# Kernel tuning notes

Measured on AMD Instinct MI355X. Metric: run time of the kernel, lower is better.

The kernel has to match this reference:

```python
import jax, jax.numpy as jnp
import numpy as np

N_POINTS = 300000
NUM_CLUSTERS = 64
LATENT_DIM = 32
DET = 1e-16  # matches `det` in update_gamma


def setup_inputs() -> dict:
    key = jax.random.key(0)
    k1, k2, k3 = jax.random.split(key, 3)
    mu_phi = jax.random.normal(k1, (N_POINTS, LATENT_DIM), dtype=jnp.float32)
    # per-node scalar log-variance (encoder's gcn_logstddev has output dim 1)
    log_cov_phi = jax.random.normal(k2, (N_POINTS, 1), dtype=jnp.float32) * 0.1
    pi_k = jnp.ones((NUM_CLUSTERS,), jnp.float32) / NUM_CLUSTERS
    mu_k = jax.random.normal(k3, (NUM_CLUSTERS, LATENT_DIM), dtype=jnp.float32)
    log_cov_k = jnp.full((NUM_CLUSTERS, 1), 0.1, jnp.float32)
    return {"mu_phi": mu_phi, "log_cov_phi": log_cov_phi, "pi_k": pi_k,
            "mu_k": mu_k, "log_cov_k": log_cov_k, "P": LATENT_DIM}


def _sq_dist(a, b):
    # ||a_i - b_k||^2 via expansion; avoids materializing [N,K,P]
    return (jnp.sum(a * a, axis=1)[:, None]
            - 2.0 * (a @ b.T)
            + jnp.sum(b * b, axis=1)[None, :])


def reference(mu_phi, log_cov_phi, pi_k, mu_k, log_cov_k, P):
    Pf = jnp.float32(P)
    lcp = log_cov_phi[:, 0]          # [N]
    lck = log_cov_k[:, 0]            # [K]
    # --- update_gamma: KL[i,k] between q(z_i) and cluster k (isotropic) ---
    sq = _sq_dist(mu_phi, mu_k)      # [N,K]
    inv_cov_k = jnp.exp(-lck)[None, :]
    KL = 0.5 * (Pf * (lck[None, :] - lcp[:, None]) - Pf
                + Pf * jnp.exp(lcp)[:, None] * inv_cov_k
                + sq * inv_cov_k)    # [N,K]
    w = pi_k[None, :] * jnp.exp(-KL)
    gamma = w / jnp.sum(w, axis=1, keepdims=True) + DET  # [N,K]
    # --- update_others: M-step using the new gamma ---
    N_k = jnp.sum(gamma, axis=0)                          # [K]
    pi_new = N_k / jnp.float32(gamma.shape[0])
    mu_new = (gamma.T @ mu_phi) / N_k[:, None]            # [K,P]
    sq2 = _sq_dist(mu_phi, mu_new)                        # [N,K]
    diff = Pf * jnp.exp(lcp)[:, None] + sq2               # [N,K]
    cov_new = jnp.sum(gamma * diff, axis=0) / (Pf * N_k)  # [K]
    log_cov_new = jnp.log(cov_new)[:, None]               # [K,1]
    return gamma, pi_new, mu_new, log_cov_new
```

## Files before the change

### kernel.cpp

```cpp
#include <hip/hip_runtime.h>
#include <math.h>

#define NPTS 300000
#define K 64
#define P 32
#define DETC 1e-16f
#define WS_FLOATS (K + K + K * P)

#define NTHREADS 256
#define WPB (NTHREADS / 64)
#define NTILES ((NPTS + 63) / 64)
#define NBLOCKS ((NTILES + WPB - 1) / WPB)

#define DPP_ADD(v, ctrl)                                                     \
    v += __int_as_float(__builtin_amdgcn_update_dpp(                         \
        0, __float_as_int(v), (ctrl), 0xF, 0xF, true))

__device__ __forceinline__ float rlf(float x, int l) {
    return __int_as_float(__builtin_amdgcn_readlane(__float_as_int(x), l));
}

__device__ __forceinline__ float wave_sum64(float w) {
    float v = w;
    DPP_ADD(v, 0xB1);
    DPP_ADD(v, 0x4E);
    DPP_ADD(v, 0x128);
    DPP_ADD(v, 0x124);
    DPP_ADD(v, 0x142);
    DPP_ADD(v, 0x143);
    return rlf(v, 63);
}

__global__ __launch_bounds__(NTHREADS, 4) void em_pass(
    const float* __restrict__ mu_phi,
    const float* __restrict__ log_cov_phi,
    const float* __restrict__ pi_k,
    const float* __restrict__ mu_k,
    const float* __restrict__ log_cov_k,
    float* __restrict__ gamma_out,
    float* __restrict__ out_tail,
    float* __restrict__ ws)
{
    const int lane = threadIdx.x & 63;
    const int wave = threadIdx.x >> 6;
    const int tile = __builtin_amdgcn_readfirstlane(blockIdx.x * WPB + wave);

    float muk[P];
#pragma unroll
    for (int d = 0; d < P; ++d) muk[d] = mu_k[lane * P + d];
    const float lck  = log_cov_k[lane];
    const float icov = __expf(-lck);
    const float pik  = pi_k[lane];
    float n2k = 0.f;
#pragma unroll
    for (int d = 0; d < P; ++d) n2k = fmaf(muk[d], muk[d], n2k);
    const float Ak    = 0.5f * (32.f * lck - 32.f + icov * n2k) - __logf(pik);
    const float hicov = 0.5f * icov;

    float accN = 0.f, accS = 0.f;
    float accM[P];
#pragma unroll
    for (int d = 0; d < P; ++d) accM[d] = 0.f;

    if (tile < NTILES) {
        const int gb  = tile * 64;
        const int cnt = (NPTS - gb < 64) ? (NPTS - gb) : 64;

        const int ip = gb + ((lane < cnt) ? lane : (cnt - 1));
        float r[P];
        {
            const float4* r4 = reinterpret_cast<const float4*>(mu_phi + (size_t)ip * P);
            float4 a0 = r4[0], a1 = r4[1], a2 = r4[2], a3 = r4[3];
            float4 a4 = r4[4], a5 = r4[5], a6 = r4[6], a7 = r4[7];
#define PUT(j,q) r[4*j+0]=q.x; r[4*j+1]=q.y; r[4*j+2]=q.z; r[4*j+3]=q.w
            PUT(0,a0); PUT(1,a1); PUT(2,a2); PUT(3,a3);
            PUT(4,a4); PUT(5,a5); PUT(6,a6); PUT(7,a7);
#undef PUT
        }
        float n2 = 0.f;
#pragma unroll
        for (int d = 0; d < P; ++d) n2 = fmaf(r[d], r[d], n2);
        const float lcp = log_cov_phi[ip];
        const float u_v = fmaf(32.f, __expf(lcp), n2);
        const float b_v = 16.f * lcp;

        for (int p = 0; p < cnt; ++p) {
            float sr[P];
#pragma unroll
            for (int d = 0; d < P; ++d) sr[d] = rlf(r[d], p);

            float d0 = 0.f, d1 = 0.f, d2 = 0.f, d3 = 0.f;
#pragma unroll
            for (int d = 0; d < P; d += 4) {
                d0 = fmaf(sr[d + 0], muk[d + 0], d0);
                d1 = fmaf(sr[d + 1], muk[d + 1], d1);
                d2 = fmaf(sr[d + 2], muk[d + 2], d2);
                d3 = fmaf(sr[d + 3], muk[d + 3], d3);
            }
            const float dot = (d0 + d1) + (d2 + d3);

            const float u_s = rlf(u_v, p);
            const float b_s = rlf(b_v, p);
            const float t = fmaf(-hicov, u_s, b_s) - Ak;
            const float w = __expf(fmaf(icov, dot, t));

            const float s = wave_sum64(w);
            const float g = fmaf(w, __builtin_amdgcn_rcpf(s), DETC);
            gamma_out[(size_t)(gb + p) * K + lane] = g;

            accN += g;
            accS = fmaf(g, u_s, accS);
#pragma unroll
            for (int d = 0; d < P; ++d) accM[d] = fmaf(g, sr[d], accM[d]);
        }
    }

    __shared__ float lN[K], lS[K], lM[K * P];
    for (int idx = threadIdx.x; idx < K; idx += NTHREADS) { lN[idx] = 0.f; lS[idx] = 0.f; }
    for (int idx = threadIdx.x; idx < K * P; idx += NTHREADS) lM[idx] = 0.f;
    __syncthreads();

    atomicAdd(&lN[lane], accN);
    atomicAdd(&lS[lane], accS);
#pragma unroll
    for (int d = 0; d < P; ++d) atomicAdd(&lM[d * K + lane], accM[d]);
    __syncthreads();

    for (int idx = threadIdx.x; idx < K; idx += NTHREADS) {
        atomicAdd(&ws[idx], lN[idx]);
        atomicAdd(&ws[K + idx], lS[idx]);
    }
    for (int idx = threadIdx.x; idx < K * P; idx += NTHREADS)
        atomicAdd(&ws[2 * K + idx], lM[idx]);
    __syncthreads();

    __shared__ int lastf;
    if (threadIdx.x == 0) {
        __threadfence();
        const int c = atomicAdd((int*)(ws + WS_FLOATS), 1);
        lastf = (c == NBLOCKS - 1);
    }
    __syncthreads();
    if (lastf) {
        __threadfence();
        const int k = threadIdx.x;
        if (k < K) {
            const float Nk = __hip_atomic_load(&ws[k],     __ATOMIC_RELAXED, __HIP_MEMORY_SCOPE_AGENT);
            const float S  = __hip_atomic_load(&ws[K + k], __ATOMIC_RELAXED, __HIP_MEMORY_SCOPE_AGENT);
            float* pi_new      = out_tail;
            float* mu_new      = out_tail + K;
            float* log_cov_new = out_tail + K + K * P;

            pi_new[k] = Nk / (float)NPTS;
            const float invN = 1.f / Nk;
            float m2 = 0.f;
#pragma unroll
            for (int d = 0; d < P; ++d) {
                const float md = __hip_atomic_load(&ws[2 * K + d * K + k],
                                                   __ATOMIC_RELAXED, __HIP_MEMORY_SCOPE_AGENT) * invN;
                mu_new[k * P + d] = md;
                m2 = fmaf(md, md, m2);
            }
            const float cov = (S - Nk * m2) / (32.f * Nk);
            log_cov_new[k] = logf(cov);
        }
    }
}

extern "C" void kernel_launch(void* const* d_in, const int* in_sizes, int n_in,
                              void* d_out, int out_size, void* d_ws, size_t ws_size,
                              hipStream_t stream)
{
    const float* mu_phi      = (const float*)d_in[0];
    const float* log_cov_phi = (const float*)d_in[1];
    const float* pi_k        = (const float*)d_in[2];
    const float* mu_k        = (const float*)d_in[3];
    const float* log_cov_k   = (const float*)d_in[4];
    float* out = (float*)d_out;
    float* ws  = (float*)d_ws;

    hipMemsetAsync(ws, 0, (WS_FLOATS + 1) * sizeof(float), stream);
    em_pass<<<NBLOCKS, NTHREADS, 0, stream>>>(mu_phi, log_cov_phi, pi_k, mu_k,
                                              log_cov_k, out,
                                              out + (size_t)NPTS * K, ws);
}
```

Measured before the change: 216.2 us.

## Map one point per lane and transpose gamma through LDS for M-step accumulation

Each lane now owns one data point and loops over all 64 clusters, reading cluster means as wave-uniform values. This removes the per-point readlane broadcasts and the 64-lane DPP reduction of the old cluster-per-lane scheme. Gamma and the point features are staged in per-wave LDS and read back transposed, so each lane accumulates the N_k, covariance and mean sums for one cluster over half the points. The exponent is rewritten as a single exp2, and occupancy is lowered to 2 waves per SIMD to make room for the larger register footprint (w[64], accM[32]).

```diff
diff --git a/kernel.cpp b/kernel.cpp
--- a/kernel.cpp
+++ b/kernel.cpp
@@ -8,30 +8,27 @@
 #define WS_FLOATS (K + K + K * P)
 
 #define NTHREADS 256
-#define WPB (NTHREADS / 64)
+#define WPB 4
 #define NTILES ((NPTS + 63) / 64)
 #define NBLOCKS ((NTILES + WPB - 1) / WPB)
 
-#define DPP_ADD(v, ctrl)                                                     \
-    v += __int_as_float(__builtin_amdgcn_update_dpp(                         \
-        0, __float_as_int(v), (ctrl), 0xF, 0xF, true))
+#define PHS 36
+#define GS  33
+#define WAVE_LDS (64 * PHS + 64 * GS)
+#define COMB_OFF (WPB * WAVE_LDS)
+#define TOTAL_LDS (COMB_OFF + WS_FLOATS)
+
+#if __has_builtin(__builtin_amdgcn_exp2f)
+#define EXP2(x) __builtin_amdgcn_exp2f(x)
+#else
+#define EXP2(x) __exp2f(x)
+#endif
 
 __device__ __forceinline__ float rlf(float x, int l) {
     return __int_as_float(__builtin_amdgcn_readlane(__float_as_int(x), l));
 }
 
-__device__ __forceinline__ float wave_sum64(float w) {
-    float v = w;
-    DPP_ADD(v, 0xB1);
-    DPP_ADD(v, 0x4E);
-    DPP_ADD(v, 0x128);
-    DPP_ADD(v, 0x124);
-    DPP_ADD(v, 0x142);
-    DPP_ADD(v, 0x143);
-    return rlf(v, 63);
-}
-
-__global__ __launch_bounds__(NTHREADS, 4) void em_pass(
+__global__ __launch_bounds__(NTHREADS, 2) void em_pass(
     const float* __restrict__ mu_phi,
     const float* __restrict__ log_cov_phi,
     const float* __restrict__ pi_k,
@@ -41,104 +38,146 @@
     float* __restrict__ out_tail,
     float* __restrict__ ws)
 {
+    __shared__ float smem[TOTAL_LDS];
+    __shared__ int lastf;
+
     const int lane = threadIdx.x & 63;
     const int wave = threadIdx.x >> 6;
     const int tile = __builtin_amdgcn_readfirstlane(blockIdx.x * WPB + wave);
 
-    float muk[P];
-#pragma unroll
-    for (int d = 0; d < P; ++d) muk[d] = mu_k[lane * P + d];
-    const float lck  = log_cov_k[lane];
-    const float icov = __expf(-lck);
-    const float pik  = pi_k[lane];
-    float n2k = 0.f;
-#pragma unroll
-    for (int d = 0; d < P; ++d) n2k = fmaf(muk[d], muk[d], n2k);
-    const float Ak    = 0.5f * (32.f * lck - 32.f + icov * n2k) - __logf(pik);
-    const float hicov = 0.5f * icov;
-
-    float accN = 0.f, accS = 0.f;
+    float* phiT = smem + wave * WAVE_LDS;
+    float* G    = phiT + 64 * PHS;
+    float* comb = smem + COMB_OFF;
+
+    const float LOG2E = 1.4426950408889634f;
+
+    float icL, c2L;
+    {
+        const float4* mk4 = reinterpret_cast<const float4*>(mu_k + lane * P);
+        float n2k = 0.f;
+#pragma unroll
+        for (int q = 0; q < 8; ++q) {
+            float4 v = mk4[q];
+            n2k = fmaf(v.x, v.x, n2k); n2k = fmaf(v.y, v.y, n2k);
+            n2k = fmaf(v.z, v.z, n2k); n2k = fmaf(v.w, v.w, n2k);
+        }
+        const float lck  = log_cov_k[lane];
+        const float icov = __expf(-lck);
+        const float pik  = pi_k[lane];
+        const float C = fmaf(-0.5f * icov, n2k, 16.f - 16.f * lck) + __logf(pik);
+        icL = icov * LOG2E;
+        c2L = C * LOG2E;
+    }
+
+    for (int idx = threadIdx.x; idx < WS_FLOATS; idx += NTHREADS) comb[idx] = 0.f;
+    __syncthreads();
+
+    const int gb  = tile * 64;
+    const int cnt = (NPTS - gb < 64) ? (NPTS - gb) : 64;
+
+    const int ip = gb + ((lane < cnt) ? lane : (cnt - 1));
+    float r[P];
+    {
+        const float4* r4 = reinterpret_cast<const float4*>(mu_phi + (size_t)ip * P);
+#pragma unroll
+        for (int q = 0; q < 8; ++q) {
+            float4 v = r4[q];
+            r[4*q+0] = v.x; r[4*q+1] = v.y; r[4*q+2] = v.z; r[4*q+3] = v.w;
+        }
+    }
+    float n2 = 0.f;
+#pragma unroll
+    for (int d = 0; d < P; ++d) n2 = fmaf(r[d], r[d], n2);
+    const float lcp = log_cov_phi[ip];
+    const float u   = fmaf(32.f, __expf(lcp), n2);
+    const float b2  = 16.f * LOG2E * lcp;
+    const float hu  = 0.5f * u;
+
+    {
+        float4* prow = reinterpret_cast<float4*>(phiT + lane * PHS);
+#pragma unroll
+        for (int q = 0; q < 8; ++q)
+            prow[q] = make_float4(r[4*q+0], r[4*q+1], r[4*q+2], r[4*q+3]);
+        phiT[lane * PHS + 32] = u;
+    }
+
+    float w[K];
+    float S = 0.f;
+#pragma unroll
+    for (int k = 0; k < K; ++k) {
+        const float* mk = mu_k + k * P;
+        float d0 = 0.f, d1 = 0.f, d2 = 0.f, d3 = 0.f;
+#pragma unroll
+        for (int d = 0; d < P; d += 4) {
+            d0 = fmaf(mk[d + 0], r[d + 0], d0);
+            d1 = fmaf(mk[d + 1], r[d + 1], d1);
+            d2 = fmaf(mk[d + 2], r[d + 2], d2);
+            d3 = fmaf(mk[d + 3], r[d + 3], d3);
+        }
+        const float dot = (d0 + d1) + (d2 + d3);
+        const float ic2 = rlf(icL, k);
+        const float bC  = b2 + rlf(c2L, k);
+        const float E   = fmaf(ic2, dot - hu, bC);
+        const float wk  = EXP2(E);
+        w[k] = wk;
+        S += wk;
+    }
+    const float rcpS = __builtin_amdgcn_rcpf(S);
+
+    float accN = 0.f, accSv = 0.f;
     float accM[P];
-#pragma unroll
-    for (int d = 0; d < P; ++d) accM[d] = 0.f;
-
-    if (tile < NTILES) {
-        const int gb  = tile * 64;
-        const int cnt = (NPTS - gb < 64) ? (NPTS - gb) : 64;
-
-        const int ip = gb + ((lane < cnt) ? lane : (cnt - 1));
-        float r[P];
-        {
-            const float4* r4 = reinterpret_cast<const float4*>(mu_phi + (size_t)ip * P);
-            float4 a0 = r4[0], a1 = r4[1], a2 = r4[2], a3 = r4[3];
-            float4 a4 = r4[4], a5 = r4[5], a6 = r4[6], a7 = r4[7];
-#define PUT(j,q) r[4*j+0]=q.x; r[4*j+1]=q.y; r[4*j+2]=q.z; r[4*j+3]=q.w
-            PUT(0,a0); PUT(1,a1); PUT(2,a2); PUT(3,a3);
-            PUT(4,a4); PUT(5,a5); PUT(6,a6); PUT(7,a7);
-#undef PUT
-        }
-        float n2 = 0.f;
-#pragma unroll
-        for (int d = 0; d < P; ++d) n2 = fmaf(r[d], r[d], n2);
-        const float lcp = log_cov_phi[ip];
-        const float u_v = fmaf(32.f, __expf(lcp), n2);
-        const float b_v = 16.f * lcp;
-
-        for (int p = 0; p < cnt; ++p) {
-            float sr[P];
-#pragma unroll
-            for (int d = 0; d < P; ++d) sr[d] = rlf(r[d], p);
-
-            float d0 = 0.f, d1 = 0.f, d2 = 0.f, d3 = 0.f;
-#pragma unroll
-            for (int d = 0; d < P; d += 4) {
-                d0 = fmaf(sr[d + 0], muk[d + 0], d0);
-                d1 = fmaf(sr[d + 1], muk[d + 1], d1);
-                d2 = fmaf(sr[d + 2], muk[d + 2], d2);
-                d3 = fmaf(sr[d + 3], muk[d + 3], d3);
+    const int hh = lane >> 5;
+    const int jj = lane & 31;
+
+#pragma unroll
+    for (int c = 0; c < 2; ++c) {
+#pragma unroll
+        for (int j = 0; j < 32; ++j)
+            G[lane * GS + j] = fmaf(w[c * 32 + j], rcpS, DETC);
+
+        accN = 0.f; accSv = 0.f;
+#pragma unroll
+        for (int d = 0; d < P; ++d) accM[d] = 0.f;
+
+        for (int pp = 0; pp < 32; ++pp) {
+            const int p = hh * 32 + pp;
+            const bool valid = (p < cnt);
+            const float gval = G[p * GS + jj];
+            const float uu   = phiT[p * PHS + 32];
+            const float g    = valid ? gval : 0.f;
+            if (valid)
+                gamma_out[(size_t)(gb + p) * K + c * 32 + jj] = gval;
+            accN  += g;
+            accSv  = fmaf(g, uu, accSv);
+            const float4* pr = reinterpret_cast<const float4*>(phiT + p * PHS);
+#pragma unroll
+            for (int q = 0; q < 8; ++q) {
+                float4 v = pr[q];
+                accM[4*q+0] = fmaf(g, v.x, accM[4*q+0]);
+                accM[4*q+1] = fmaf(g, v.y, accM[4*q+1]);
+                accM[4*q+2] = fmaf(g, v.z, accM[4*q+2]);
+                accM[4*q+3] = fmaf(g, v.w, accM[4*q+3]);
             }
-            const float dot = (d0 + d1) + (d2 + d3);
-
-            const float u_s = rlf(u_v, p);
-            const float b_s = rlf(b_v, p);
-            const float t = fmaf(-hicov, u_s, b_s) - Ak;
-            const float w = __expf(fmaf(icov, dot, t));
-
-            const float s = wave_sum64(w);
-            const float g = fmaf(w, __builtin_amdgcn_rcpf(s), DETC);
-            gamma_out[(size_t)(gb + p) * K + lane] = g;
-
-            accN += g;
-            accS = fmaf(g, u_s, accS);
-#pragma unroll
-            for (int d = 0; d < P; ++d) accM[d] = fmaf(g, sr[d], accM[d]);
-        }
-    }
-
-    __shared__ float lN[K], lS[K], lM[K * P];
-    for (int idx = threadIdx.x; idx < K; idx += NTHREADS) { lN[idx] = 0.f; lS[idx] = 0.f; }
-    for (int idx = threadIdx.x; idx < K * P; idx += NTHREADS) lM[idx] = 0.f;
-    __syncthreads();
-
-    atomicAdd(&lN[lane], accN);
-    atomicAdd(&lS[lane], accS);
-#pragma unroll
-    for (int d = 0; d < P; ++d) atomicAdd(&lM[d * K + lane], accM[d]);
-    __syncthreads();
-
-    for (int idx = threadIdx.x; idx < K; idx += NTHREADS) {
-        atomicAdd(&ws[idx], lN[idx]);
-        atomicAdd(&ws[K + idx], lS[idx]);
-    }
-    for (int idx = threadIdx.x; idx < K * P; idx += NTHREADS)
-        atomicAdd(&ws[2 * K + idx], lM[idx]);
-    __syncthreads();
-
-    __shared__ int lastf;
+        }
+
+        const int kk = c * 32 + jj;
+        atomicAdd(&comb[kk], accN);
+        atomicAdd(&comb[K + kk], accSv);
+#pragma unroll
+        for (int d = 0; d < P; ++d)
+            atomicAdd(&comb[2 * K + d * K + kk], accM[d]);
+    }
+
+    __syncthreads();
+
+    for (int idx = threadIdx.x; idx < WS_FLOATS; idx += NTHREADS)
+        atomicAdd(&ws[idx], comb[idx]);
+    __syncthreads();
+
     if (threadIdx.x == 0) {
         __threadfence();
-        const int c = atomicAdd((int*)(ws + WS_FLOATS), 1);
-        lastf = (c == NBLOCKS - 1);
+        const int cdone = atomicAdd((int*)(ws + WS_FLOATS), 1);
+        lastf = (cdone == NBLOCKS - 1);
     }
     __syncthreads();
     if (lastf) {
@@ -146,7 +185,7 @@
         const int k = threadIdx.x;
         if (k < K) {
             const float Nk = __hip_atomic_load(&ws[k],     __ATOMIC_RELAXED, __HIP_MEMORY_SCOPE_AGENT);
-            const float S  = __hip_atomic_load(&ws[K + k], __ATOMIC_RELAXED, __HIP_MEMORY_SCOPE_AGENT);
+            const float Sk = __hip_atomic_load(&ws[K + k], __ATOMIC_RELAXED, __HIP_MEMORY_SCOPE_AGENT);
             float* pi_new      = out_tail;
             float* mu_new      = out_tail + K;
             float* log_cov_new = out_tail + K + K * P;
@@ -161,7 +200,7 @@
                 mu_new[k * P + d] = md;
                 m2 = fmaf(md, md, m2);
             }
-            const float cov = (S - Nk * m2) / (32.f * Nk);
+            const float cov = (Sk - Nk * m2) / (32.f * Nk);
             log_cov_new[k] = logf(cov);
         }
     }
```

Result: slower. 293.9 us (+35.9%).
